# Optimization experiments

Hardware: AMD Instinct MI355X
Metric: run time of the kernel (lower is better)

Reference implementation:

```python
import jax, jax.numpy as jnp
import numpy as np

B, S, I, H = 64, 512, 1024, 1024


def setup_inputs() -> dict:
    key = jax.random.key(0)
    ks = jax.random.split(key, 7)
    sc = 0.02
    return {
        "x": jax.random.normal(ks[0], (B, S, I), jnp.float32),
        "Wx0": jax.random.normal(ks[1], (I, 4 * H), jnp.float32) * sc,
        "Wh0": jax.random.normal(ks[2], (H, 4 * H), jnp.float32) * sc,
        "b0": jax.random.normal(ks[3], (4 * H,), jnp.float32) * sc,
        "Wx1": jax.random.normal(ks[4], (H, 4 * H), jnp.float32) * sc,
        "Wh1": jax.random.normal(ks[5], (H, 4 * H), jnp.float32) * sc,
        "b1": jax.random.normal(ks[6], (4 * H,), jnp.float32) * sc,
    }


def _lstm_layer(x_seq, Wx, Wh, b):
    """x_seq: (S, B, in). Gate order along 4H axis: i, f, g, o."""
    hid = Wh.shape[0]
    # Precompute input-side projections for all timesteps (one big GEMM).
    xg = jnp.einsum('sbi,ih->sbh', x_seq, Wx) + b  # (S, B, 4H)

    def step(carry, xg_t):
        h, c = carry
        g = xg_t + h @ Wh                      # (B, 4H)
        i, f, gg, o = jnp.split(g, 4, axis=-1)
        i = jax.nn.sigmoid(i)
        f = jax.nn.sigmoid(f)
        gg = jnp.tanh(gg)
        o = jax.nn.sigmoid(o)
        c = f * c + i * gg
        h = o * jnp.tanh(c)
        return (h, c), h

    bsz = x_seq.shape[1]
    h0 = jnp.zeros((bsz, hid), x_seq.dtype)
    c0 = jnp.zeros((bsz, hid), x_seq.dtype)
    (_, _), hs = jax.lax.scan(step, (h0, c0), xg)
    return hs  # (S, B, H)


def reference(x, Wx0, Wh0, b0, Wx1, Wh1, b1):
    # batch_first=True -> (B,S,I); internal layout is time-major (S,B,I)
    xs = jnp.swapaxes(x, 0, 1)
    h1 = _lstm_layer(xs, Wx0, Wh0, b0)
    h2 = _lstm_layer(h1, Wx1, Wh1, b1)
    return jnp.swapaxes(h2, 0, 1)  # (B, S, H)
```

## Files before the change

kernel.cpp:

```cpp
#include <hip/hip_runtime.h>
#include <hip/hip_bf16.h>

#define SEQ  512
#define HID  1024
#define G4   4096
#define NBLK 128

typedef short bf16x8 __attribute__((ext_vector_type(8)));
typedef float f32x4  __attribute__((ext_vector_type(4)));
typedef unsigned long long u64;

static __device__ __forceinline__ unsigned short f2b(float f) {
  union { float f; unsigned u; } v; v.f = f;
  unsigned r = (v.u + 0x7FFFu + ((v.u >> 16) & 1u)) >> 16;
  return (unsigned short)r;
}

__global__ __launch_bounds__(256) void k_castx(const float* __restrict__ x,
                                               unsigned short* __restrict__ xb) {
  int idx = blockIdx.x * 256 + threadIdx.x;
  int r = idx >> 8, kq = idx & 255;
  int b = r & 63, s = r >> 6;
  float4 v = *reinterpret_cast<const float4*>(x + ((size_t)b * SEQ + s) * HID + (size_t)kq * 4);
  ushort4 o;
  o.x = f2b(v.x); o.y = f2b(v.y); o.z = f2b(v.z); o.w = f2b(v.w);
  *reinterpret_cast<ushort4*>(xb + (size_t)r * HID + kq * 4) = o;
}

__global__ __launch_bounds__(256) void k_wtrans(const float* __restrict__ W,
                                                unsigned short* __restrict__ WT) {
  __shared__ float tls[32][33];
  int tile = blockIdx.x;
  int nt = tile & 127, kt = tile >> 7;
  int tx = threadIdx.x & 31, ty = threadIdx.x >> 5;
  int k0 = kt * 32, n0 = nt * 32;
  for (int i = 0; i < 4; ++i)
    tls[ty + 8 * i][tx] = W[(size_t)(k0 + ty + 8 * i) * G4 + n0 + tx];
  __syncthreads();
  for (int i = 0; i < 4; ++i)
    WT[(size_t)(n0 + ty + 8 * i) * HID + k0 + tx] = f2b(tls[tx][ty + 8 * i]);
}

static __device__ __forceinline__ void wait_ge(unsigned* p, unsigned tgt) {
  long sp = 0;
  while (__hip_atomic_load(p, __ATOMIC_RELAXED, __HIP_MEMORY_SCOPE_AGENT) < tgt) {
    if (++sp > 8000000L) break;
    __builtin_amdgcn_s_sleep(1);
  }
  asm volatile("" ::: "memory");
}

__global__ __launch_bounds__(512, 1) void k_scan2(
    const unsigned short* __restrict__ xb,
    const unsigned short* __restrict__ WxT0, const unsigned short* __restrict__ WhT0,
    const float* __restrict__ b0,
    const unsigned short* __restrict__ WxT1, const unsigned short* __restrict__ WhT1,
    const float* __restrict__ b1,
    unsigned short* __restrict__ h1,
    unsigned short* __restrict__ h2, int h2mod,
    float* __restrict__ out,
    unsigned* __restrict__ bars) {
  __shared__ unsigned short wlds[32 * 2048];
  __shared__ float g_lds[2][64][35];
  __shared__ unsigned lds_arr;

  const int bk  = blockIdx.x;
  const int layer = bk >> 7;
  const int nb  = bk & 127;
  const int tid = threadIdx.x;
  const int w   = tid >> 6;
  const int l   = tid & 63;
  const int lq  = l >> 4, lr = l & 15;
  const int rt  = w & 3;
  const bool is_h = (w >= 4);

  const unsigned short* WxT = layer ? WxT1 : WxT0;
  const unsigned short* WhT = layer ? WhT1 : WhT0;
  const float* bias = layer ? b1 : b0;
  const unsigned short* aseq = layer ? h1 : xb;
  unsigned short* hout = layer ? h2 : h1;
  const int hmod = layer ? h2mod : 512;
  float* fout = layer ? out : nullptr;
  unsigned* ownc = bars + layer * 32;
  unsigned* l0c  = bars;

  if (tid == 0) lds_arr = 0;

  {
    int c = tid >> 4, seg = tid & 15;
    int gate = c >> 3, nl = c & 7;
    int gcol = gate * 1024 + nb * 8 + nl;
    const unsigned short* sx = WxT + (size_t)gcol * HID;
    const unsigned short* sh = WhT + (size_t)gcol * HID;
    for (int j = 0; j < 16; ++j) {
      int kk = seg * 128 + j * 8;
      const unsigned short* src = (kk < 1024) ? (sx + kk) : (sh + kk - 1024);
      uint4 v = *reinterpret_cast<const uint4*>(src);
      int db = (c * 4096 + kk * 2) ^ ((c & 7) << 4);
      *reinterpret_cast<uint4*>(reinterpret_cast<char*>(wlds) + db) = v;
    }
  }

  char* wbase = reinterpret_cast<char*>(wlds);
  const int csw = (lr & 7) << 4;
  const int cb0 = (lr) * 4096 + lq * 16;
  const int cb1 = (16 + lr) * 4096 + lq * 16;

  float bias_c[2];
#pragma unroll
  for (int ct = 0; ct < 2; ++ct) {
    int col = ct * 16 + lr;
    bias_c[ct] = bias[(col >> 3) * 1024 + nb * 8 + (col & 7)];
  }

  const int eb = rt * 16 + (l >> 2);
  const int np = l & 3;
  const int hcol = nb * 8 + 2 * np;
  float cA = 0.f, cB = 0.f;

  __syncthreads();
  if (is_h) __builtin_amdgcn_s_setprio(1);

  if (!is_h) {
    if (layer) wait_ge(l0c, NBLK);
    const bf16x8* ax = reinterpret_cast<const bf16x8*>(aseq) + (size_t)(rt * 16 + lr) * 128 + lq;
    f32x4 acc[2][4] = {};
#pragma unroll 8
    for (int ks = 0; ks < 32; ++ks) {
      bf16x8 a  = ax[ks * 4];
      bf16x8 bb0 = *reinterpret_cast<const bf16x8*>(wbase + ((cb0 + ks * 64) ^ csw));
      bf16x8 bb1 = *reinterpret_cast<const bf16x8*>(wbase + ((cb1 + ks * 64) ^ csw));
      acc[0][ks & 3] = __builtin_amdgcn_mfma_f32_16x16x32_bf16(a, bb0, acc[0][ks & 3], 0, 0, 0);
      acc[1][ks & 3] = __builtin_amdgcn_mfma_f32_16x16x32_bf16(a, bb1, acc[1][ks & 3], 0, 0, 0);
    }
#pragma unroll
    for (int ct = 0; ct < 2; ++ct) {
      f32x4 s = (acc[ct][0] + acc[ct][1]) + (acc[ct][2] + acc[ct][3]);
      int row = rt * 16 + lq * 4, col = ct * 16 + lr;
      g_lds[0][row + 0][col] = s.x + bias_c[ct];
      g_lds[0][row + 1][col] = s.y + bias_c[ct];
      g_lds[0][row + 2][col] = s.z + bias_c[ct];
      g_lds[0][row + 3][col] = s.w + bias_c[ct];
    }
  }
  __syncthreads();

  for (int t = 0; t < SEQ; ++t) {
    if (!is_h) {
      if (t + 1 < SEQ) {
        if (layer) wait_ge(l0c, (unsigned)(t + 2) * NBLK);
        const bf16x8* ax = reinterpret_cast<const bf16x8*>(aseq)
                           + ((size_t)(t + 1) * 64 + rt * 16 + lr) * 128 + lq;
        f32x4 acc[2][4] = {};
#pragma unroll 8
        for (int ks = 0; ks < 32; ++ks) {
          bf16x8 a  = ax[ks * 4];
          bf16x8 bb0 = *reinterpret_cast<const bf16x8*>(wbase + ((cb0 + ks * 64) ^ csw));
          bf16x8 bb1 = *reinterpret_cast<const bf16x8*>(wbase + ((cb1 + ks * 64) ^ csw));
          acc[0][ks & 3] = __builtin_amdgcn_mfma_f32_16x16x32_bf16(a, bb0, acc[0][ks & 3], 0, 0, 0);
          acc[1][ks & 3] = __builtin_amdgcn_mfma_f32_16x16x32_bf16(a, bb1, acc[1][ks & 3], 0, 0, 0);
        }
        int bn = (t + 1) & 1;
#pragma unroll
        for (int ct = 0; ct < 2; ++ct) {
          f32x4 s = (acc[ct][0] + acc[ct][1]) + (acc[ct][2] + acc[ct][3]);
          int row = rt * 16 + lq * 4, col = ct * 16 + lr;
          g_lds[bn][row + 0][col] = s.x + bias_c[ct];
          g_lds[bn][row + 1][col] = s.y + bias_c[ct];
          g_lds[bn][row + 2][col] = s.z + bias_c[ct];
          g_lds[bn][row + 3][col] = s.w + bias_c[ct];
        }
      }
    } else {
      if (t > 0) {
        wait_ge(ownc, (unsigned)t * NBLK);
        const size_t hbase = (size_t)((t - 1) % hmod) * (64 * HID) + (size_t)(rt * 16 + lr) * HID;
        f32x4 acc[2][4] = {};
        if (hmod != 4) {
          const bf16x8* hp = reinterpret_cast<const bf16x8*>(hout + hbase) + lq;
#pragma unroll 8
          for (int ks = 0; ks < 32; ++ks) {
            bf16x8 a = hp[ks * 4];
            bf16x8 bb0 = *reinterpret_cast<const bf16x8*>(wbase + ((cb0 + 2048 + ks * 64) ^ csw));
            bf16x8 bb1 = *reinterpret_cast<const bf16x8*>(wbase + ((cb1 + 2048 + ks * 64) ^ csw));
            acc[0][ks & 3] = __builtin_amdgcn_mfma_f32_16x16x32_bf16(a, bb0, acc[0][ks & 3], 0, 0, 0);
            acc[1][ks & 3] = __builtin_amdgcn_mfma_f32_16x16x32_bf16(a, bb1, acc[1][ks & 3], 0, 0, 0);
          }
        } else {
          const u64* hp = reinterpret_cast<const u64*>(hout + hbase) + lq * 2;
#pragma unroll 8
          for (int ks = 0; ks < 32; ++ks) {
            u64 q0 = __hip_atomic_load(hp + ks * 8,     __ATOMIC_RELAXED, __HIP_MEMORY_SCOPE_AGENT);
            u64 q1 = __hip_atomic_load(hp + ks * 8 + 1, __ATOMIC_RELAXED, __HIP_MEMORY_SCOPE_AGENT);
            union { u64 q[2]; bf16x8 v; } u; u.q[0] = q0; u.q[1] = q1;
            bf16x8 bb0 = *reinterpret_cast<const bf16x8*>(wbase + ((cb0 + 2048 + ks * 64) ^ csw));
            bf16x8 bb1 = *reinterpret_cast<const bf16x8*>(wbase + ((cb1 + 2048 + ks * 64) ^ csw));
            acc[0][ks & 3] = __builtin_amdgcn_mfma_f32_16x16x32_bf16(u.v, bb0, acc[0][ks & 3], 0, 0, 0);
            acc[1][ks & 3] = __builtin_amdgcn_mfma_f32_16x16x32_bf16(u.v, bb1, acc[1][ks & 3], 0, 0, 0);
          }
        }
        int bn = t & 1;
#pragma unroll
        for (int ct = 0; ct < 2; ++ct) {
          f32x4 s = (acc[ct][0] + acc[ct][1]) + (acc[ct][2] + acc[ct][3]);
          int row = rt * 16 + lq * 4, col = ct * 16 + lr;
          g_lds[bn][row + 0][col] += s.x;
          g_lds[bn][row + 1][col] += s.y;
          g_lds[bn][row + 2][col] += s.z;
          g_lds[bn][row + 3][col] += s.w;
        }
      }

      {
        int bn = t & 1;
        float hv[2];
#pragma unroll
        for (int cv = 0; cv < 2; ++cv) {
          int c = 2 * np + cv;
          float gi = g_lds[bn][eb][c];
          float gf = g_lds[bn][eb][8 + c];
          float gg = g_lds[bn][eb][16 + c];
          float go = g_lds[bn][eb][24 + c];
          float ig = 1.f / (1.f + __expf(-gi));
          float fg = 1.f / (1.f + __expf(-gf));
          float e2 = __expf(2.f * gg);
          float gv = (e2 - 1.f) / (e2 + 1.f);
          float og = 1.f / (1.f + __expf(-go));
          float& cst = cv ? cB : cA;
          cst = fg * cst + ig * gv;
          float e2c = __expf(2.f * cst);
          hv[cv] = og * (e2c - 1.f) / (e2c + 1.f);
        }
        unsigned packed = (unsigned)f2b(hv[0]) | ((unsigned)f2b(hv[1]) << 16);
        unsigned* hw = reinterpret_cast<unsigned*>(
            hout + (size_t)(t % hmod) * (64 * HID) + (size_t)eb * HID + hcol);
        __hip_atomic_store(hw, packed, __ATOMIC_RELAXED, __HIP_MEMORY_SCOPE_AGENT);
        if (fout)
          *reinterpret_cast<float2*>(fout + (size_t)eb * (SEQ * HID) + (size_t)t * HID + hcol) =
              make_float2(hv[0], hv[1]);
      }

      asm volatile("s_waitcnt vmcnt(0)" ::: "memory");
      if (l == 0) {
        unsigned pb = atomicAdd(&lds_arr, 1u);
        if ((pb & 3) == 3)
          __hip_atomic_fetch_add(ownc, 1u, __ATOMIC_RELAXED, __HIP_MEMORY_SCOPE_AGENT);
      }
    }
    __syncthreads();
  }
}

extern "C" void kernel_launch(void* const* d_in, const int* in_sizes, int n_in,
                              void* d_out, int out_size, void* d_ws, size_t ws_size,
                              hipStream_t stream) {
  const float* x   = (const float*)d_in[0];
  const float* Wx0 = (const float*)d_in[1];
  const float* Wh0 = (const float*)d_in[2];
  const float* b0  = (const float*)d_in[3];
  const float* Wx1 = (const float*)d_in[4];
  const float* Wh1 = (const float*)d_in[5];
  const float* b1  = (const float*)d_in[6];
  float* out = (float*)d_out;
  char* ws = (char*)d_ws;

  unsigned short* xb   = (unsigned short*)(ws);
  unsigned short* h1   = (unsigned short*)(ws + 67108864);
  unsigned short* WxT0 = (unsigned short*)(ws + 134217728);
  unsigned short* WhT0 = (unsigned short*)(ws + 142606336);
  unsigned short* WxT1 = (unsigned short*)(ws + 150994944);
  unsigned short* WhT1 = (unsigned short*)(ws + 159383552);
  unsigned* bars       = (unsigned*)(ws + 167772160);
  unsigned short* h2   = (unsigned short*)(ws + 167776256);
  int h2mod = (ws_size >= (size_t)167776256 + 67108864) ? 512 : 4;

  hipMemsetAsync(bars, 0, 4096, stream);
  k_castx<<<32768, 256, 0, stream>>>(x, xb);
  k_wtrans<<<4096, 256, 0, stream>>>(Wx0, WxT0);
  k_wtrans<<<4096, 256, 0, stream>>>(Wh0, WhT0);
  k_wtrans<<<4096, 256, 0, stream>>>(Wx1, WxT1);
  k_wtrans<<<4096, 256, 0, stream>>>(Wh1, WhT1);
  k_scan2<<<2 * NBLK, 512, 0, stream>>>(xb, WxT0, WhT0, b0, WxT1, WhT1, b1,
                                        h1, h2, h2mod, out, bars);
}
```

Baseline: 5.440 ms.

## Shard barrier counters, use leader-wave polling, and compute gates in registers

Splits the single global step counter into eight group counters, 128 bytes apart, and polls them in parallel with a wave-wide vote. This cuts atomic contention on one address. One wave per role now polls global memory and signals the other waves through an LDS flag, and the gate nonlinearities are computed straight from MFMA accumulators using lane shuffles instead of a round-trip through a shared gate buffer. The risks are a higher register count, extra spinning in the LDS flag waits, and a layout change in the bars workspace that must match the launcher's zeroing.

```diff
diff --git a/kernel.cpp b/kernel.cpp
--- a/kernel.cpp
+++ b/kernel.cpp
@@ -41,10 +41,22 @@
     WT[(size_t)(n0 + ty + 8 * i) * HID + k0 + tx] = f2b(tls[tx][ty + 8 * i]);
 }
 
-static __device__ __forceinline__ void wait_ge(unsigned* p, unsigned tgt) {
+static __device__ __forceinline__ void wave_wait8(unsigned* base, unsigned tgt) {
+  unsigned* p = base + (threadIdx.x & 7) * 32;
   long sp = 0;
-  while (__hip_atomic_load(p, __ATOMIC_RELAXED, __HIP_MEMORY_SCOPE_AGENT) < tgt) {
-    if (++sp > 8000000L) break;
+  for (;;) {
+    unsigned v = __hip_atomic_load(p, __ATOMIC_RELAXED, __HIP_MEMORY_SCOPE_AGENT);
+    if (__all(v >= tgt)) break;
+    if (++sp > 10000000L) break;
+    __builtin_amdgcn_s_sleep(1);
+  }
+  asm volatile("" ::: "memory");
+}
+
+static __device__ __forceinline__ void lds_wait(int* f, int tgt) {
+  long sp = 0;
+  while (__hip_atomic_load(f, __ATOMIC_RELAXED, __HIP_MEMORY_SCOPE_WORKGROUP) < tgt) {
+    if (++sp > 200000000L) break;
     __builtin_amdgcn_s_sleep(1);
   }
   asm volatile("" ::: "memory");
@@ -61,8 +73,9 @@
     float* __restrict__ out,
     unsigned* __restrict__ bars) {
   __shared__ unsigned short wlds[32 * 2048];
-  __shared__ float g_lds[2][64][35];
+  __shared__ float x_lds[2][4][8][64];
   __shared__ unsigned lds_arr;
+  __shared__ int hrdy, xrdy;
 
   const int bk  = blockIdx.x;
   const int layer = bk >> 7;
@@ -81,10 +94,10 @@
   unsigned short* hout = layer ? h2 : h1;
   const int hmod = layer ? h2mod : 512;
   float* fout = layer ? out : nullptr;
-  unsigned* ownc = bars + layer * 32;
-  unsigned* l0c  = bars;
-
-  if (tid == 0) lds_arr = 0;
+  unsigned* ownbase = bars + layer * 256;
+  unsigned* grpc = ownbase + (nb >> 4) * 32;
+
+  if (tid == 0) { lds_arr = 0; hrdy = 0; xrdy = 0; }
 
   {
     int c = tid >> 4, seg = tid & 15;
@@ -113,16 +126,13 @@
     bias_c[ct] = bias[(col >> 3) * 1024 + nb * 8 + (col & 7)];
   }
 
-  const int eb = rt * 16 + (l >> 2);
-  const int np = l & 3;
-  const int hcol = nb * 8 + 2 * np;
-  float cA = 0.f, cB = 0.f;
+  float cst[4] = {0.f, 0.f, 0.f, 0.f};
 
   __syncthreads();
   if (is_h) __builtin_amdgcn_s_setprio(1);
 
   if (!is_h) {
-    if (layer) wait_ge(l0c, NBLK);
+    if (layer) wave_wait8(bars, 16u);
     const bf16x8* ax = reinterpret_cast<const bf16x8*>(aseq) + (size_t)(rt * 16 + lr) * 128 + lq;
     f32x4 acc[2][4] = {};
 #pragma unroll 8
@@ -136,11 +146,11 @@
 #pragma unroll
     for (int ct = 0; ct < 2; ++ct) {
       f32x4 s = (acc[ct][0] + acc[ct][1]) + (acc[ct][2] + acc[ct][3]);
-      int row = rt * 16 + lq * 4, col = ct * 16 + lr;
-      g_lds[0][row + 0][col] = s.x + bias_c[ct];
-      g_lds[0][row + 1][col] = s.y + bias_c[ct];
-      g_lds[0][row + 2][col] = s.z + bias_c[ct];
-      g_lds[0][row + 3][col] = s.w + bias_c[ct];
+      float bc = bias_c[ct];
+      x_lds[0][w][ct * 4 + 0][l] = s.x + bc;
+      x_lds[0][w][ct * 4 + 1][l] = s.y + bc;
+      x_lds[0][w][ct * 4 + 2][l] = s.z + bc;
+      x_lds[0][w][ct * 4 + 3][l] = s.w + bc;
     }
   }
   __syncthreads();
@@ -148,7 +158,14 @@
   for (int t = 0; t < SEQ; ++t) {
     if (!is_h) {
       if (t + 1 < SEQ) {
-        if (layer) wait_ge(l0c, (unsigned)(t + 2) * NBLK);
+        if (layer) {
+          if (w == 0) {
+            wave_wait8(bars, 16u * (unsigned)(t + 2));
+            __hip_atomic_store(&xrdy, t + 1, __ATOMIC_RELAXED, __HIP_MEMORY_SCOPE_WORKGROUP);
+          } else {
+            lds_wait(&xrdy, t + 1);
+          }
+        }
         const bf16x8* ax = reinterpret_cast<const bf16x8*>(aseq)
                            + ((size_t)(t + 1) * 64 + rt * 16 + lr) * 128 + lq;
         f32x4 acc[2][4] = {};
@@ -160,22 +177,37 @@
           acc[0][ks & 3] = __builtin_amdgcn_mfma_f32_16x16x32_bf16(a, bb0, acc[0][ks & 3], 0, 0, 0);
           acc[1][ks & 3] = __builtin_amdgcn_mfma_f32_16x16x32_bf16(a, bb1, acc[1][ks & 3], 0, 0, 0);
         }
-        int bn = (t + 1) & 1;
+        int bn2 = (t + 1) & 1;
 #pragma unroll
         for (int ct = 0; ct < 2; ++ct) {
           f32x4 s = (acc[ct][0] + acc[ct][1]) + (acc[ct][2] + acc[ct][3]);
-          int row = rt * 16 + lq * 4, col = ct * 16 + lr;
-          g_lds[bn][row + 0][col] = s.x + bias_c[ct];
-          g_lds[bn][row + 1][col] = s.y + bias_c[ct];
-          g_lds[bn][row + 2][col] = s.z + bias_c[ct];
-          g_lds[bn][row + 3][col] = s.w + bias_c[ct];
+          float bc = bias_c[ct];
+          x_lds[bn2][w][ct * 4 + 0][l] = s.x + bc;
+          x_lds[bn2][w][ct * 4 + 1][l] = s.y + bc;
+          x_lds[bn2][w][ct * 4 + 2][l] = s.z + bc;
+          x_lds[bn2][w][ct * 4 + 3][l] = s.w + bc;
         }
       }
     } else {
+      const int bn = t & 1;
+      f32x4 acc[2][4];
+#pragma unroll
+      for (int ct = 0; ct < 2; ++ct) {
+        acc[ct][0] = f32x4{x_lds[bn][rt][ct * 4 + 0][l], x_lds[bn][rt][ct * 4 + 1][l],
+                           x_lds[bn][rt][ct * 4 + 2][l], x_lds[bn][rt][ct * 4 + 3][l]};
+        acc[ct][1] = f32x4{0.f, 0.f, 0.f, 0.f};
+        acc[ct][2] = f32x4{0.f, 0.f, 0.f, 0.f};
+        acc[ct][3] = f32x4{0.f, 0.f, 0.f, 0.f};
+      }
+
       if (t > 0) {
-        wait_ge(ownc, (unsigned)t * NBLK);
+        if (w == 4) {
+          wave_wait8(ownbase, 16u * (unsigned)t);
+          __hip_atomic_store(&hrdy, t, __ATOMIC_RELAXED, __HIP_MEMORY_SCOPE_WORKGROUP);
+        } else {
+          lds_wait(&hrdy, t);
+        }
         const size_t hbase = (size_t)((t - 1) % hmod) * (64 * HID) + (size_t)(rt * 16 + lr) * HID;
-        f32x4 acc[2][4] = {};
         if (hmod != 4) {
           const bf16x8* hp = reinterpret_cast<const bf16x8*>(hout + hbase) + lq;
 #pragma unroll 8
@@ -199,52 +231,65 @@
             acc[1][ks & 3] = __builtin_amdgcn_mfma_f32_16x16x32_bf16(u.v, bb1, acc[1][ks & 3], 0, 0, 0);
           }
         }
-        int bn = t & 1;
-#pragma unroll
-        for (int ct = 0; ct < 2; ++ct) {
-          f32x4 s = (acc[ct][0] + acc[ct][1]) + (acc[ct][2] + acc[ct][3]);
-          int row = rt * 16 + lq * 4, col = ct * 16 + lr;
-          g_lds[bn][row + 0][col] += s.x;
-          g_lds[bn][row + 1][col] += s.y;
-          g_lds[bn][row + 2][col] += s.z;
-          g_lds[bn][row + 3][col] += s.w;
-        }
-      }
-
-      {
-        int bn = t & 1;
-        float hv[2];
-#pragma unroll
-        for (int cv = 0; cv < 2; ++cv) {
-          int c = 2 * np + cv;
-          float gi = g_lds[bn][eb][c];
-          float gf = g_lds[bn][eb][8 + c];
-          float gg = g_lds[bn][eb][16 + c];
-          float go = g_lds[bn][eb][24 + c];
-          float ig = 1.f / (1.f + __expf(-gi));
-          float fg = 1.f / (1.f + __expf(-gf));
-          float e2 = __expf(2.f * gg);
-          float gv = (e2 - 1.f) / (e2 + 1.f);
-          float og = 1.f / (1.f + __expf(-go));
-          float& cst = cv ? cB : cA;
-          cst = fg * cst + ig * gv;
-          float e2c = __expf(2.f * cst);
-          hv[cv] = og * (e2c - 1.f) / (e2c + 1.f);
-        }
-        unsigned packed = (unsigned)f2b(hv[0]) | ((unsigned)f2b(hv[1]) << 16);
-        unsigned* hw = reinterpret_cast<unsigned*>(
-            hout + (size_t)(t % hmod) * (64 * HID) + (size_t)eb * HID + hcol);
-        __hip_atomic_store(hw, packed, __ATOMIC_RELAXED, __HIP_MEMORY_SCOPE_AGENT);
-        if (fout)
-          *reinterpret_cast<float2*>(fout + (size_t)eb * (SEQ * HID) + (size_t)t * HID + hcol) =
-              make_float2(hv[0], hv[1]);
+      }
+
+      f32x4 s0 = (acc[0][0] + acc[0][1]) + (acc[0][2] + acc[0][3]);
+      f32x4 s1 = (acc[1][0] + acc[1][1]) + (acc[1][2] + acc[1][3]);
+      float a0[4] = {s0.x, s0.y, s0.z, s0.w};
+      float a1[4] = {s1.x, s1.y, s1.z, s1.w};
+      float b0r[4], b1r[4];
+#pragma unroll
+      for (int r = 0; r < 4; ++r) {
+        b0r[r] = __shfl_xor(a0[r], 8, 64);
+        b1r[r] = __shfl_xor(a1[r], 8, 64);
+      }
+      const bool isX = ((l & 8) == 0);
+      float hvf[4];
+#pragma unroll
+      for (int r = 0; r < 4; ++r) {
+        float gi = isX ? a0[r] : b0r[r];
+        float gf = isX ? b0r[r] : a0[r];
+        float gg = isX ? a1[r] : b1r[r];
+        float go = isX ? b1r[r] : a1[r];
+        float ig = 1.f / (1.f + __expf(-gi));
+        float fg = 1.f / (1.f + __expf(-gf));
+        float e2 = __expf(2.f * gg);
+        float gv = (e2 - 1.f) / (e2 + 1.f);
+        float og = 1.f / (1.f + __expf(-go));
+        cst[r] = fg * cst[r] + ig * gv;
+        float e2c = __expf(2.f * cst[r]);
+        hvf[r] = og * (e2c - 1.f) / (e2c + 1.f);
+      }
+      float hn[4];
+#pragma unroll
+      for (int r = 0; r < 4; ++r) hn[r] = __shfl_xor(hvf[r], 1, 64);
+      const bool ev = ((l & 1) == 0);
+      unsigned pk[4]; float he[4], ho[4];
+#pragma unroll
+      for (int r = 0; r < 4; ++r) {
+        he[r] = ev ? hvf[r] : hn[r];
+        ho[r] = ev ? hn[r] : hvf[r];
+        pk[r] = (unsigned)f2b(he[r]) | ((unsigned)f2b(ho[r]) << 16);
+      }
+      const int sub = ((l >> 3) & 1) * 2 + (l & 1);
+      unsigned pks = sub == 0 ? pk[0] : sub == 1 ? pk[1] : sub == 2 ? pk[2] : pk[3];
+      const int row = rt * 16 + lq * 4 + sub;
+      const int cp  = (lr & 7) >> 1;
+      unsigned* hw = reinterpret_cast<unsigned*>(hout + (size_t)(t % hmod) * (64 * HID))
+                     + (size_t)row * 512 + nb * 4 + cp;
+      __hip_atomic_store(hw, pks, __ATOMIC_RELAXED, __HIP_MEMORY_SCOPE_AGENT);
+      if (fout) {
+        float hes = sub == 0 ? he[0] : sub == 1 ? he[1] : sub == 2 ? he[2] : he[3];
+        float hos = sub == 0 ? ho[0] : sub == 1 ? ho[1] : sub == 2 ? ho[2] : ho[3];
+        *reinterpret_cast<float2*>(fout + (size_t)row * (SEQ * HID) + (size_t)t * HID
+                                   + nb * 8 + cp * 2) = make_float2(hes, hos);
       }
 
       asm volatile("s_waitcnt vmcnt(0)" ::: "memory");
       if (l == 0) {
         unsigned pb = atomicAdd(&lds_arr, 1u);
         if ((pb & 3) == 3)
-          __hip_atomic_fetch_add(ownc, 1u, __ATOMIC_RELAXED, __HIP_MEMORY_SCOPE_AGENT);
+          __hip_atomic_fetch_add(grpc, 1u, __ATOMIC_RELAXED, __HIP_MEMORY_SCOPE_AGENT);
       }
     }
     __syncthreads();
```

Result: faster. 5.081 ms (-6.6%).
